# Kernel optimization log

Hardware: AMD Instinct MI355X
Metric: run time of the kernel (lower is better)

## Reference

```python
import jax, jax.numpy as jnp
import numpy as np

DM, DFF = 128, 512          # d_model, d_ff = 4*d_model
B, D, L, FACTOR = 8, 64, 256, 10  # batch, ts_d, seg_num, router factor


def _ln(x, g, b):
    m = jnp.mean(x, axis=-1, keepdims=True)
    v = jnp.mean(jnp.square(x - m), axis=-1, keepdims=True)
    return (x - m) * jax.lax.rsqrt(v + 1e-5) * g + b


def _mlp(x, W1, b1, W2, b2):
    # nn.Linear -> GELU(exact/erf, torch default) -> nn.Linear
    return jax.nn.gelu(x @ W1 + b1, approximate=False) @ W2 + b2


def setup_inputs():
    key = jax.random.key(0)
    ks = jax.random.split(key, 9)
    f32 = jnp.float32
    return {
        "x": jax.random.normal(ks[0], (B, D, L, DM), f32),
        "router": jax.random.normal(ks[1], (L, FACTOR, DM), f32),
        # out_projection biases of the three AutoCorrelationLayers
        "bo_time": jax.random.normal(ks[2], (DM,), f32) * 0.02,
        "bo_send": jax.random.normal(ks[3], (DM,), f32) * 0.02,
        "bo_recv": jax.random.normal(ks[4], (DM,), f32) * 0.02,
        "g1": jnp.ones((DM,), f32), "be1": jnp.zeros((DM,), f32),
        "g2": jnp.ones((DM,), f32), "be2": jnp.zeros((DM,), f32),
        "g3": jnp.ones((DM,), f32), "be3": jnp.zeros((DM,), f32),
        "g4": jnp.ones((DM,), f32), "be4": jnp.zeros((DM,), f32),
        "W1a": jax.random.normal(ks[5], (DM, DFF), f32) * 0.02, "b1a": jnp.zeros((DFF,), f32),
        "W2a": jax.random.normal(ks[6], (DFF, DM), f32) * 0.02, "b2a": jnp.zeros((DM,), f32),
        "W1b": jax.random.normal(ks[7], (DM, DFF), f32) * 0.02, "b1b": jnp.zeros((DFF,), f32),
        "W2b": jax.random.normal(ks[8], (DFF, DM), f32) * 0.02, "b2b": jnp.zeros((DM,), f32),
    }


def reference(x, router, bo_time, bo_send, bo_recv, g1, be1, g2, be2, g3, be3, g4, be4,
              W1a, b1a, W2a, b2a, W1b, b1b, W2b, b2b):
    b, d, l, dm = x.shape
    time_in = x.reshape(b * d, l, dm)
    # FourierBlock is constructed with modes=0 -> get_frequency_modes returns an
    # EMPTY index set -> out_ft stays all-zero -> irfft(0) == 0. Therefore every
    # AutoCorrelationLayer output is exactly its out_projection bias broadcast;
    # the Q/K/V/out weights, bo_send and the router are dead w.r.t. the output
    # (zero gradient). Dropout is identity in eval mode.
    dim_in = _ln(time_in + bo_time, g1, be1)                            # residual + norm1
    dim_in = _ln(dim_in + _mlp(dim_in, W1a, b1a, W2a, b2a), g2, be2)    # MLP1 + norm2
    # '(b d) l dm -> (b l) d dm'
    dim_send = dim_in.reshape(b, d, l, dm).transpose(0, 2, 1, 3).reshape(b * l, d, dm)
    dim_enc = _ln(dim_send + bo_recv, g3, be3)                          # dim_receiver bias + norm3
    dim_enc = _ln(dim_enc + _mlp(dim_enc, W1b, b1b, W2b, b2b), g4, be4) # MLP2 + norm4
    # '(b l) d dm -> b d l dm'
    return dim_enc.reshape(b, l, d, dm).transpose(0, 2, 1, 3)
```

## Files before the change

kernel.cpp:

```cpp
#include <hip/hip_runtime.h>
#include <hip/hip_fp16.h>

typedef _Float16 f16;
typedef f16 f16x8 __attribute__((ext_vector_type(8)));
typedef f16 f16x2 __attribute__((ext_vector_type(2)));
typedef float f32x4 __attribute__((ext_vector_type(4)));

__device__ __align__(16) f16 g_wimg[524288];

#define RSTRIDE 528

__device__ __forceinline__ float gelu_f(float x) {
  float z = fabsf(x) * 0.70710678118654752f;
  float t = __builtin_amdgcn_rcpf(fmaf(0.3275911f, z, 1.0f));
  float p = fmaf(1.061405429f, t, -1.453152027f);
  p = fmaf(p, t, 1.421413741f);
  p = fmaf(p, t, -0.284496736f);
  p = fmaf(p, t, 0.254829592f);
  p = p * t;
  float e = __expf(-z * z);
  float er = fmaf(-p, e, 1.0f);
  er = copysignf(er, x);
  return 0.5f * x * (1.0f + er);
}

__global__ __launch_bounds__(256) void prep_weights(
    const float* __restrict__ W1a, const float* __restrict__ W2a,
    const float* __restrict__ W1b, const float* __restrict__ W2b) {
  int p = blockIdx.x * 256 + threadIdx.x;
  int mat = p >> 16;
  int rem = p & 65535;
  int plane = rem >> 15;
  int rem2 = rem & 32767;
  int frag = rem2 >> 8;
  int q = rem2 & 255;
  int lane = q >> 2;
  int j = (q & 3) * 2;
  int chunk = frag >> 5;
  int cb = (frag >> 2) & 7;
  int ks = frag & 3;
  int l15 = lane & 15, l4 = lane >> 4;
  int col16 = cb * 16 + l15;
  int kk = ks * 32 + l4 * 8 + j;
  const float* W = (mat == 0) ? W1a : (mat == 1) ? W2a : (mat == 2) ? W1b : W2b;
  float s0, s1;
  if ((mat & 1) == 0) {
    int colg = chunk * 128 + col16;
    s0 = W[kk * 512 + colg];
    s1 = W[(kk + 1) * 512 + colg];
  } else {
    int kg = chunk * 128 + kk;
    s0 = W[kg * 128 + col16];
    s1 = W[(kg + 1) * 128 + col16];
  }
  f16x2 h;
  if (plane == 0) {
    h.x = (f16)s0;
    h.y = (f16)s1;
  } else {
    h.x = (f16)(s0 - (float)(f16)s0);
    h.y = (f16)(s1 - (float)(f16)s1);
  }
  *(f16x2*)((unsigned char*)g_wimg + mat * 262144 + plane * 131072 +
            frag * 1024 + lane * 16 + j * 2) = h;
}

__device__ __forceinline__ void split8(const float4& a, const float4& b,
                                       f16x8& h, f16x8& l) {
  float v[8] = {a.x, a.y, a.z, a.w, b.x, b.y, b.z, b.w};
#pragma unroll
  for (int j = 0; j < 8; ++j) {
    f16 x = (f16)v[j];
    h[j] = x;
    l[j] = (f16)(v[j] - (float)x);
  }
}

__device__ __forceinline__ void mlp_stage(
    char* scr, const f16x8 (&bfh)[4], const f16x8 (&bfl)[4], f32x4 (&zacc)[8],
    const f16* __restrict__ W1img, const f16* __restrict__ W2img,
    const float* __restrict__ b1, int lane, int l15, int l4) {
  for (int chunk = 0; chunk < 4; ++chunk) {
#pragma unroll
    for (int m = 0; m < 8; ++m) {
      f32x4 t4 = {0.f, 0.f, 0.f, 0.f};
#pragma unroll
      for (int ks = 0; ks < 4; ++ks) {
        int frag = (chunk * 8 + m) * 4 + ks;
        f16x8 wh = *(const f16x8*)(W1img + frag * 512 + lane * 8);
        f16x8 wl = *(const f16x8*)(W1img + 65536 + frag * 512 + lane * 8);
        t4 = __builtin_amdgcn_mfma_f32_16x16x32_f16(wh, bfh[ks], t4, 0, 0, 0);
        t4 = __builtin_amdgcn_mfma_f32_16x16x32_f16(wl, bfh[ks], t4, 0, 0, 0);
        t4 = __builtin_amdgcn_mfma_f32_16x16x32_f16(wh, bfl[ks], t4, 0, 0, 0);
      }
      float4 bv = *(const float4*)(b1 + chunk * 128 + m * 16 + l4 * 4);
      float4 g;
      g.x = gelu_f(t4[0] + bv.x);
      g.y = gelu_f(t4[1] + bv.y);
      g.z = gelu_f(t4[2] + bv.z);
      g.w = gelu_f(t4[3] + bv.w);
      *(float4*)(scr + l15 * RSTRIDE + m * 64 + l4 * 16) = g;
    }
#pragma unroll
    for (int ks = 0; ks < 4; ++ks) {
      const char* hb = scr + l15 * RSTRIDE + ks * 128 + l4 * 32;
      float4 h0 = *(const float4*)(hb);
      float4 h1 = *(const float4*)(hb + 16);
      f16x8 ah, al;
      split8(h0, h1, ah, al);
#pragma unroll
      for (int n = 0; n < 8; ++n) {
        int frag = (chunk * 8 + n) * 4 + ks;
        f16x8 bh = *(const f16x8*)(W2img + frag * 512 + lane * 8);
        f16x8 bl = *(const f16x8*)(W2img + 65536 + frag * 512 + lane * 8);
        zacc[n] = __builtin_amdgcn_mfma_f32_16x16x32_f16(ah, bh, zacc[n], 0, 0, 0);
        zacc[n] = __builtin_amdgcn_mfma_f32_16x16x32_f16(al, bh, zacc[n], 0, 0, 0);
        zacc[n] = __builtin_amdgcn_mfma_f32_16x16x32_f16(ah, bl, zacc[n], 0, 0, 0);
      }
    }
  }
}

#define ROW_LN_STATS(ZACC, MMV, RSV)                                   \
  float MMV[4], RSV[4];                                                \
  _Pragma("unroll") for (int r = 0; r < 4; ++r) {                      \
    float s = 0.f, q = 0.f;                                            \
    _Pragma("unroll") for (int n = 0; n < 8; ++n) {                    \
      float v = ZACC[n][r];                                            \
      s += v;                                                          \
      q += v * v;                                                      \
    }                                                                  \
    _Pragma("unroll") for (int m = 8; m >= 1; m >>= 1) {               \
      s += __shfl_xor(s, m, 64);                                       \
      q += __shfl_xor(q, m, 64);                                       \
    }                                                                  \
    float mm = s * (1.f / 128.f);                                      \
    float var = q * (1.f / 128.f) - mm * mm;                           \
    MMV[r] = mm;                                                       \
    RSV[r] = rsqrtf(var + 1e-5f);                                      \
  }

__global__ __launch_bounds__(256, 2) void tsal_kernel(
    const float* __restrict__ x,
    const float* __restrict__ bo_time, const float* __restrict__ bo_recv,
    const float* __restrict__ g1, const float* __restrict__ be1,
    const float* __restrict__ g2, const float* __restrict__ be2,
    const float* __restrict__ g3, const float* __restrict__ be3,
    const float* __restrict__ g4, const float* __restrict__ be4,
    const float* __restrict__ b1a, const float* __restrict__ b2a,
    const float* __restrict__ b1b, const float* __restrict__ b2b,
    float* __restrict__ out) {
  __shared__ __align__(16) char smem[33792];

  const int tid = threadIdx.x;
  const int lane = tid & 63;
  const int wv = tid >> 6;
  const int l15 = lane & 15, l4 = lane >> 4;
  char* scr = smem + wv * 8448;
  const int R0 = blockIdx.x * 64 + wv * 16;

#pragma unroll
  for (int it = 0; it < 8; ++it) {
    int rl = it * 2 + (lane >> 5);
    int c0 = (lane & 31) * 4;
    float4 xv = *(const float4*)(x + (size_t)(R0 + rl) * 128 + c0);
    float4 bt = *(const float4*)(bo_time + c0);
    float vx = xv.x + bt.x, vy = xv.y + bt.y, vz = xv.z + bt.z, vw = xv.w + bt.w;
    float s = vx + vy + vz + vw;
    float q = vx * vx + vy * vy + vz * vz + vw * vw;
#pragma unroll
    for (int m = 16; m >= 1; m >>= 1) {
      s += __shfl_xor(s, m, 64);
      q += __shfl_xor(q, m, 64);
    }
    float mm = s * (1.f / 128.f);
    float rs = rsqrtf(q * (1.f / 128.f) - mm * mm + 1e-5f);
    float4 gv = *(const float4*)(g1 + c0);
    float4 bv = *(const float4*)(be1 + c0);
    float4 w;
    w.x = (vx - mm) * rs * gv.x + bv.x;
    w.y = (vy - mm) * rs * gv.y + bv.y;
    w.z = (vz - mm) * rs * gv.z + bv.z;
    w.w = (vw - mm) * rs * gv.w + bv.w;
    *(float4*)(scr + rl * RSTRIDE + c0 * 4) = w;
  }

  f16x8 bfh[4], bfl[4];
#pragma unroll
  for (int ks = 0; ks < 4; ++ks) {
    const char* wb = scr + l15 * RSTRIDE + ks * 128 + l4 * 32;
    float4 a0 = *(const float4*)(wb);
    float4 a1 = *(const float4*)(wb + 16);
    split8(a0, a1, bfh[ks], bfl[ks]);
  }
  f32x4 zacc[8];
#pragma unroll
  for (int n = 0; n < 8; ++n)
#pragma unroll
    for (int r = 0; r < 4; ++r)
      zacc[n][r] = *(const float*)(scr + (l4 * 4 + r) * RSTRIDE +
                                   (n * 16 + l15) * 4);

  mlp_stage(scr, bfh, bfl, zacc, g_wimg, g_wimg + 131072, b1a, lane, l15, l4);

  float b2v[8], g2v[8], be2v[8], brv[8], g3v[8], be3v[8];
#pragma unroll
  for (int n = 0; n < 8; ++n) {
    int col = n * 16 + l15;
    b2v[n] = b2a[col];
    g2v[n] = g2[col];
    be2v[n] = be2[col];
    brv[n] = bo_recv[col];
    g3v[n] = g3[col];
    be3v[n] = be3[col];
  }
#pragma unroll
  for (int n = 0; n < 8; ++n)
#pragma unroll
    for (int r = 0; r < 4; ++r) zacc[n][r] += b2v[n];
  {
    ROW_LN_STATS(zacc, mm2, rs2)
#pragma unroll
    for (int n = 0; n < 8; ++n)
#pragma unroll
      for (int r = 0; r < 4; ++r)
        zacc[n][r] = (zacc[n][r] - mm2[r]) * rs2[r] * g2v[n] + be2v[n] + brv[n];
  }
  {
    ROW_LN_STATS(zacc, mm3, rs3)
#pragma unroll
    for (int n = 0; n < 8; ++n)
#pragma unroll
      for (int r = 0; r < 4; ++r)
        zacc[n][r] = (zacc[n][r] - mm3[r]) * rs3[r] * g3v[n] + be3v[n];
  }
#pragma unroll
  for (int n = 0; n < 8; ++n)
#pragma unroll
    for (int r = 0; r < 4; ++r)
      *(float*)(scr + (l4 * 4 + r) * RSTRIDE + (n * 16 + l15) * 4) =
          zacc[n][r];
#pragma unroll
  for (int ks = 0; ks < 4; ++ks) {
    const char* yb = scr + l15 * RSTRIDE + ks * 128 + l4 * 32;
    float4 a0 = *(const float4*)(yb);
    float4 a1 = *(const float4*)(yb + 16);
    split8(a0, a1, bfh[ks], bfl[ks]);
  }

  mlp_stage(scr, bfh, bfl, zacc, g_wimg + 262144, g_wimg + 393216, b1b, lane,
            l15, l4);

  float b4v[8], g4v[8], be4v[8];
#pragma unroll
  for (int n = 0; n < 8; ++n) {
    int col = n * 16 + l15;
    b4v[n] = b2b[col];
    g4v[n] = g4[col];
    be4v[n] = be4[col];
  }
#pragma unroll
  for (int n = 0; n < 8; ++n)
#pragma unroll
    for (int r = 0; r < 4; ++r) zacc[n][r] += b4v[n];
  {
    ROW_LN_STATS(zacc, mm4, rs4)
#pragma unroll
    for (int n = 0; n < 8; ++n)
#pragma unroll
      for (int r = 0; r < 4; ++r) {
        float o = (zacc[n][r] - mm4[r]) * rs4[r] * g4v[n] + be4v[n];
        out[(size_t)(R0 + l4 * 4 + r) * 128 + n * 16 + l15] = o;
      }
  }
}

extern "C" void kernel_launch(void* const* d_in, const int* in_sizes, int n_in,
                              void* d_out, int out_size, void* d_ws, size_t ws_size,
                              hipStream_t stream) {
  const float* x = (const float*)d_in[0];
  const float* bo_time = (const float*)d_in[2];
  const float* bo_recv = (const float*)d_in[4];
  const float* g1 = (const float*)d_in[5];
  const float* be1 = (const float*)d_in[6];
  const float* g2 = (const float*)d_in[7];
  const float* be2 = (const float*)d_in[8];
  const float* g3 = (const float*)d_in[9];
  const float* be3 = (const float*)d_in[10];
  const float* g4 = (const float*)d_in[11];
  const float* be4 = (const float*)d_in[12];
  const float* b1a = (const float*)d_in[14];
  const float* b2a = (const float*)d_in[16];
  const float* b1b = (const float*)d_in[18];
  const float* b2b = (const float*)d_in[20];
  const float* W1a = (const float*)d_in[13];
  const float* W2a = (const float*)d_in[15];
  const float* W1b = (const float*)d_in[17];
  const float* W2b = (const float*)d_in[19];
  float* outp = (float*)d_out;

  int nrows = in_sizes[0] / 128;
  prep_weights<<<1024, 256, 0, stream>>>(W1a, W2a, W1b, W2b);
  tsal_kernel<<<nrows / 64, 256, 0, stream>>>(
      x, bo_time, bo_recv, g1, be1, g2, be2, g3, be3, g4, be4,
      b1a, b2a, b1b, b2b, outp);
}
```

Measured before the change: 654.7 us.

## Process two 16-row groups per wave to reuse weight fragments

```diff
diff --git a/kernel.cpp b/kernel.cpp
--- a/kernel.cpp
+++ b/kernel.cpp
@@ -9,6 +9,7 @@
 __device__ __align__(16) f16 g_wimg[524288];
 
 #define RSTRIDE 528
+#define GSTRIDE 8448
 
 __device__ __forceinline__ float gelu_f(float x) {
   float z = fabsf(x) * 0.70710678118654752f;
@@ -77,45 +78,60 @@
 }
 
 __device__ __forceinline__ void mlp_stage(
-    char* scr, const f16x8 (&bfh)[4], const f16x8 (&bfl)[4], f32x4 (&zacc)[8],
+    char* scr, const f16x8 (&bfh)[2][4], const f16x8 (&bfl)[2][4],
+    f32x4 (&zacc)[2][8],
     const f16* __restrict__ W1img, const f16* __restrict__ W2img,
     const float* __restrict__ b1, int lane, int l15, int l4) {
   for (int chunk = 0; chunk < 4; ++chunk) {
 #pragma unroll
     for (int m = 0; m < 8; ++m) {
-      f32x4 t4 = {0.f, 0.f, 0.f, 0.f};
+      f32x4 t4[2];
+      t4[0] = (f32x4){0.f, 0.f, 0.f, 0.f};
+      t4[1] = (f32x4){0.f, 0.f, 0.f, 0.f};
 #pragma unroll
       for (int ks = 0; ks < 4; ++ks) {
         int frag = (chunk * 8 + m) * 4 + ks;
         f16x8 wh = *(const f16x8*)(W1img + frag * 512 + lane * 8);
         f16x8 wl = *(const f16x8*)(W1img + 65536 + frag * 512 + lane * 8);
-        t4 = __builtin_amdgcn_mfma_f32_16x16x32_f16(wh, bfh[ks], t4, 0, 0, 0);
-        t4 = __builtin_amdgcn_mfma_f32_16x16x32_f16(wl, bfh[ks], t4, 0, 0, 0);
-        t4 = __builtin_amdgcn_mfma_f32_16x16x32_f16(wh, bfl[ks], t4, 0, 0, 0);
+#pragma unroll
+        for (int g = 0; g < 2; ++g) {
+          t4[g] = __builtin_amdgcn_mfma_f32_16x16x32_f16(wh, bfh[g][ks], t4[g], 0, 0, 0);
+          t4[g] = __builtin_amdgcn_mfma_f32_16x16x32_f16(wl, bfh[g][ks], t4[g], 0, 0, 0);
+          t4[g] = __builtin_amdgcn_mfma_f32_16x16x32_f16(wh, bfl[g][ks], t4[g], 0, 0, 0);
+        }
       }
       float4 bv = *(const float4*)(b1 + chunk * 128 + m * 16 + l4 * 4);
-      float4 g;
-      g.x = gelu_f(t4[0] + bv.x);
-      g.y = gelu_f(t4[1] + bv.y);
-      g.z = gelu_f(t4[2] + bv.z);
-      g.w = gelu_f(t4[3] + bv.w);
-      *(float4*)(scr + l15 * RSTRIDE + m * 64 + l4 * 16) = g;
+#pragma unroll
+      for (int g = 0; g < 2; ++g) {
+        float4 gg;
+        gg.x = gelu_f(t4[g][0] + bv.x);
+        gg.y = gelu_f(t4[g][1] + bv.y);
+        gg.z = gelu_f(t4[g][2] + bv.z);
+        gg.w = gelu_f(t4[g][3] + bv.w);
+        *(float4*)(scr + g * GSTRIDE + l15 * RSTRIDE + m * 64 + l4 * 16) = gg;
+      }
     }
 #pragma unroll
     for (int ks = 0; ks < 4; ++ks) {
-      const char* hb = scr + l15 * RSTRIDE + ks * 128 + l4 * 32;
-      float4 h0 = *(const float4*)(hb);
-      float4 h1 = *(const float4*)(hb + 16);
-      f16x8 ah, al;
-      split8(h0, h1, ah, al);
+      f16x8 ah[2], al[2];
+#pragma unroll
+      for (int g = 0; g < 2; ++g) {
+        const char* hb = scr + g * GSTRIDE + l15 * RSTRIDE + ks * 128 + l4 * 32;
+        float4 h0 = *(const float4*)(hb);
+        float4 h1 = *(const float4*)(hb + 16);
+        split8(h0, h1, ah[g], al[g]);
+      }
 #pragma unroll
       for (int n = 0; n < 8; ++n) {
         int frag = (chunk * 8 + n) * 4 + ks;
         f16x8 bh = *(const f16x8*)(W2img + frag * 512 + lane * 8);
         f16x8 bl = *(const f16x8*)(W2img + 65536 + frag * 512 + lane * 8);
-        zacc[n] = __builtin_amdgcn_mfma_f32_16x16x32_f16(ah, bh, zacc[n], 0, 0, 0);
-        zacc[n] = __builtin_amdgcn_mfma_f32_16x16x32_f16(al, bh, zacc[n], 0, 0, 0);
-        zacc[n] = __builtin_amdgcn_mfma_f32_16x16x32_f16(ah, bl, zacc[n], 0, 0, 0);
+#pragma unroll
+        for (int g = 0; g < 2; ++g) {
+          zacc[g][n] = __builtin_amdgcn_mfma_f32_16x16x32_f16(ah[g], bh, zacc[g][n], 0, 0, 0);
+          zacc[g][n] = __builtin_amdgcn_mfma_f32_16x16x32_f16(al[g], bh, zacc[g][n], 0, 0, 0);
+          zacc[g][n] = __builtin_amdgcn_mfma_f32_16x16x32_f16(ah[g], bl, zacc[g][n], 0, 0, 0);
+        }
       }
     }
   }
@@ -140,7 +156,7 @@
     RSV[r] = rsqrtf(var + 1e-5f);                                      \
   }
 
-__global__ __launch_bounds__(256, 2) void tsal_kernel(
+__global__ __launch_bounds__(128, 2) void tsal_kernel(
     const float* __restrict__ x,
     const float* __restrict__ bo_time, const float* __restrict__ bo_recv,
     const float* __restrict__ g1, const float* __restrict__ be1,
@@ -156,11 +172,11 @@
   const int lane = tid & 63;
   const int wv = tid >> 6;
   const int l15 = lane & 15, l4 = lane >> 4;
-  char* scr = smem + wv * 8448;
-  const int R0 = blockIdx.x * 64 + wv * 16;
-
-#pragma unroll
-  for (int it = 0; it < 8; ++it) {
+  char* scr = smem + wv * (2 * GSTRIDE);
+  const int R0 = blockIdx.x * 64 + wv * 32;
+
+#pragma unroll
+  for (int it = 0; it < 16; ++it) {
     int rl = it * 2 + (lane >> 5);
     int c0 = (lane & 31) * 4;
     float4 xv = *(const float4*)(x + (size_t)(R0 + rl) * 128 + c0);
@@ -182,24 +198,29 @@
     w.y = (vy - mm) * rs * gv.y + bv.y;
     w.z = (vz - mm) * rs * gv.z + bv.z;
     w.w = (vw - mm) * rs * gv.w + bv.w;
-    *(float4*)(scr + rl * RSTRIDE + c0 * 4) = w;
-  }
-
-  f16x8 bfh[4], bfl[4];
-#pragma unroll
-  for (int ks = 0; ks < 4; ++ks) {
-    const char* wb = scr + l15 * RSTRIDE + ks * 128 + l4 * 32;
-    float4 a0 = *(const float4*)(wb);
-    float4 a1 = *(const float4*)(wb + 16);
-    split8(a0, a1, bfh[ks], bfl[ks]);
-  }
-  f32x4 zacc[8];
-#pragma unroll
-  for (int n = 0; n < 8; ++n)
-#pragma unroll
-    for (int r = 0; r < 4; ++r)
-      zacc[n][r] = *(const float*)(scr + (l4 * 4 + r) * RSTRIDE +
-                                   (n * 16 + l15) * 4);
+    *(float4*)(scr + (rl >> 4) * GSTRIDE + (rl & 15) * RSTRIDE + c0 * 4) = w;
+  }
+
+  f16x8 bfh[2][4], bfl[2][4];
+#pragma unroll
+  for (int g = 0; g < 2; ++g)
+#pragma unroll
+    for (int ks = 0; ks < 4; ++ks) {
+      const char* wb = scr + g * GSTRIDE + l15 * RSTRIDE + ks * 128 + l4 * 32;
+      float4 a0 = *(const float4*)(wb);
+      float4 a1 = *(const float4*)(wb + 16);
+      split8(a0, a1, bfh[g][ks], bfl[g][ks]);
+    }
+  f32x4 zacc[2][8];
+#pragma unroll
+  for (int g = 0; g < 2; ++g)
+#pragma unroll
+    for (int n = 0; n < 8; ++n)
+#pragma unroll
+      for (int r = 0; r < 4; ++r)
+        zacc[g][n][r] = *(const float*)(scr + g * GSTRIDE +
+                                        (l4 * 4 + r) * RSTRIDE +
+                                        (n * 16 + l15) * 4);
 
   mlp_stage(scr, bfh, bfl, zacc, g_wimg, g_wimg + 131072, b1a, lane, l15, l4);
 
@@ -215,37 +236,41 @@
     be3v[n] = be3[col];
   }
 #pragma unroll
-  for (int n = 0; n < 8; ++n)
-#pragma unroll
-    for (int r = 0; r < 4; ++r) zacc[n][r] += b2v[n];
-  {
-    ROW_LN_STATS(zacc, mm2, rs2)
+  for (int g = 0; g < 2; ++g) {
 #pragma unroll
     for (int n = 0; n < 8; ++n)
 #pragma unroll
+      for (int r = 0; r < 4; ++r) zacc[g][n][r] += b2v[n];
+    {
+      ROW_LN_STATS(zacc[g], mm2, rs2)
+#pragma unroll
+      for (int n = 0; n < 8; ++n)
+#pragma unroll
+        for (int r = 0; r < 4; ++r)
+          zacc[g][n][r] =
+              (zacc[g][n][r] - mm2[r]) * rs2[r] * g2v[n] + be2v[n] + brv[n];
+    }
+    {
+      ROW_LN_STATS(zacc[g], mm3, rs3)
+#pragma unroll
+      for (int n = 0; n < 8; ++n)
+#pragma unroll
+        for (int r = 0; r < 4; ++r)
+          zacc[g][n][r] = (zacc[g][n][r] - mm3[r]) * rs3[r] * g3v[n] + be3v[n];
+    }
+#pragma unroll
+    for (int n = 0; n < 8; ++n)
+#pragma unroll
       for (int r = 0; r < 4; ++r)
-        zacc[n][r] = (zacc[n][r] - mm2[r]) * rs2[r] * g2v[n] + be2v[n] + brv[n];
-  }
-  {
-    ROW_LN_STATS(zacc, mm3, rs3)
-#pragma unroll
-    for (int n = 0; n < 8; ++n)
-#pragma unroll
-      for (int r = 0; r < 4; ++r)
-        zacc[n][r] = (zacc[n][r] - mm3[r]) * rs3[r] * g3v[n] + be3v[n];
-  }
-#pragma unroll
-  for (int n = 0; n < 8; ++n)
-#pragma unroll
-    for (int r = 0; r < 4; ++r)
-      *(float*)(scr + (l4 * 4 + r) * RSTRIDE + (n * 16 + l15) * 4) =
-          zacc[n][r];
-#pragma unroll
-  for (int ks = 0; ks < 4; ++ks) {
-    const char* yb = scr + l15 * RSTRIDE + ks * 128 + l4 * 32;
-    float4 a0 = *(const float4*)(yb);
-    float4 a1 = *(const float4*)(yb + 16);
-    split8(a0, a1, bfh[ks], bfl[ks]);
+        *(float*)(scr + g * GSTRIDE + (l4 * 4 + r) * RSTRIDE +
+                  (n * 16 + l15) * 4) = zacc[g][n][r];
+#pragma unroll
+    for (int ks = 0; ks < 4; ++ks) {
+      const char* yb = scr + g * GSTRIDE + l15 * RSTRIDE + ks * 128 + l4 * 32;
+      float4 a0 = *(const float4*)(yb);
+      float4 a1 = *(const float4*)(yb + 16);
+      split8(a0, a1, bfh[g][ks], bfl[g][ks]);
+    }
   }
 
   mlp_stage(scr, bfh, bfl, zacc, g_wimg + 262144, g_wimg + 393216, b1b, lane,
@@ -260,18 +285,21 @@
     be4v[n] = be4[col];
   }
 #pragma unroll
-  for (int n = 0; n < 8; ++n)
-#pragma unroll
-    for (int r = 0; r < 4; ++r) zacc[n][r] += b4v[n];
-  {
-    ROW_LN_STATS(zacc, mm4, rs4)
+  for (int g = 0; g < 2; ++g) {
 #pragma unroll
     for (int n = 0; n < 8; ++n)
 #pragma unroll
-      for (int r = 0; r < 4; ++r) {
-        float o = (zacc[n][r] - mm4[r]) * rs4[r] * g4v[n] + be4v[n];
-        out[(size_t)(R0 + l4 * 4 + r) * 128 + n * 16 + l15] = o;
-      }
+      for (int r = 0; r < 4; ++r) zacc[g][n][r] += b4v[n];
+    {
+      ROW_LN_STATS(zacc[g], mm4, rs4)
+#pragma unroll
+      for (int n = 0; n < 8; ++n)
+#pragma unroll
+        for (int r = 0; r < 4; ++r) {
+          float o = (zacc[g][n][r] - mm4[r]) * rs4[r] * g4v[n] + be4v[n];
+          out[(size_t)(R0 + g * 16 + l4 * 4 + r) * 128 + n * 16 + l15] = o;
+        }
+    }
   }
 }
 
@@ -289,19 +317,19 @@
   const float* be3 = (const float*)d_in[10];
   const float* g4 = (const float*)d_in[11];
   const float* be4 = (const float*)d_in[12];
+  const float* W1a = (const float*)d_in[13];
   const float* b1a = (const float*)d_in[14];
+  const float* W2a = (const float*)d_in[15];
   const float* b2a = (const float*)d_in[16];
+  const float* W1b = (const float*)d_in[17];
   const float* b1b = (const float*)d_in[18];
+  const float* W2b = (const float*)d_in[19];
   const float* b2b = (const float*)d_in[20];
-  const float* W1a = (const float*)d_in[13];
-  const float* W2a = (const float*)d_in[15];
-  const float* W1b = (const float*)d_in[17];
-  const float* W2b = (const float*)d_in[19];
   float* outp = (float*)d_out;
 
   int nrows = in_sizes[0] / 128;
   prep_weights<<<1024, 256, 0, stream>>>(W1a, W2a, W1b, W2b);
-  tsal_kernel<<<nrows / 64, 256, 0, stream>>>(
+  tsal_kernel<<<nrows / 64, 128, 0, stream>>>(
       x, bo_time, bo_recv, g1, be1, g2, be2, g3, be3, g4, be4,
       b1a, b2a, b1b, b2b, outp);
 }
```

After: 700.5 us. 1.07x slower.
